# Kernel optimization log

Hardware: AMD Instinct MI355X
Metric: run time of the kernel (lower is better)

The kernel has to match this reference:

```python
import jax, jax.numpy as jnp
import numpy as np

N = 100_000   # nodes
E = 1_000_000 # edges
F = 128       # nfeat
H = 2         # heads
C = 64        # nhid (per-head out channels)
NEG_SLOPE = 0.2
BN_EPS = 1e-5


def setup_inputs() -> dict:
    key = jax.random.key(0)
    ks = jax.random.split(key, 6)
    x = jax.random.normal(ks[0], (N, F), dtype=jnp.float32)
    edge_index = jax.random.randint(ks[1], (2, E), 0, N, dtype=jnp.int32)
    # GATConv params (xavier-ish scale)
    W = jax.random.normal(ks[2], (F, H * C), dtype=jnp.float32) * np.float32(1.0 / np.sqrt(F))
    att_src = jax.random.normal(ks[3], (H, C), dtype=jnp.float32) * np.float32(0.1)
    att_dst = jax.random.normal(ks[4], (H, C), dtype=jnp.float32) * np.float32(0.1)
    bias = jnp.zeros((H * C,), dtype=jnp.float32)
    # BatchNorm1d affine params
    gamma = jnp.ones((H * C,), dtype=jnp.float32)
    beta = jnp.zeros((H * C,), dtype=jnp.float32)
    return {"x": x, "edge_index": edge_index, "W": W, "att_src": att_src,
            "att_dst": att_dst, "bias": bias, "gamma": gamma, "beta": beta}


def reference(x, edge_index, W, att_src, att_dst, bias, gamma, beta):
    n = x.shape[0]
    # --- GATConv (PyG semantics): add self-loops, per-head linear, edge attention ---
    loop = jnp.arange(n, dtype=edge_index.dtype)
    src = jnp.concatenate([edge_index[0], loop])  # message sources (j)
    dst = jnp.concatenate([edge_index[1], loop])  # aggregation targets (i)

    h = (x @ W).reshape(n, H, C)                      # [N,H,C]
    a_src = jnp.einsum('nhc,hc->nh', h, att_src)      # [N,H]
    a_dst = jnp.einsum('nhc,hc->nh', h, att_dst)      # [N,H]

    e = jax.nn.leaky_relu(a_src[src] + a_dst[dst], NEG_SLOPE)  # [Et,H]
    # segment softmax over incoming edges of each dst node
    m = jax.lax.stop_gradient(jax.ops.segment_max(e, dst, num_segments=n))
    e = jnp.exp(e - m[dst])
    s = jax.ops.segment_sum(e, dst, num_segments=n)
    alpha = e / s[dst]                                 # [Et,H]

    out = jax.ops.segment_sum(alpha[:, :, None] * h[src], dst, num_segments=n)  # [N,H,C]
    out = out.reshape(n, H * C) + bias                 # concat heads + bias

    # --- transition: ReLU -> BatchNorm1d (training-mode batch stats) -> Dropout(eval=identity) ---
    out = jax.nn.relu(out)
    mean = out.mean(axis=0)
    var = out.var(axis=0)  # biased, as BN uses for normalization
    out = gamma * (out - mean) * jax.lax.rsqrt(var + BN_EPS) + beta
    return out
```

## Files before the change

### kernel.cpp

```cpp
#include <hip/hip_runtime.h>

#define NN 100000
#define EE 1000000
#define ET (EE + NN)
#define HC 128
#define NB 391
#define AGG_BLOCKS 2048
#define NGRP (NN / 4)
#define NTILE 6250
#define GEMM_BLKS 768

typedef __attribute__((ext_vector_type(8))) short short8;
typedef __attribute__((ext_vector_type(4))) float f32x4;

__device__ __forceinline__ unsigned cvtpk(float a, float b) {
    unsigned r;
    asm("v_cvt_pk_bf16_f32 %0, %1, %2" : "=v"(r) : "v"(a), "v"(b));
    return r;
}

__global__ __launch_bounds__(256) void k_gemmhist(
    const float* __restrict__ x, const float* __restrict__ W,
    const float* __restrict__ atts, const float* __restrict__ attd,
    unsigned* __restrict__ hB, float2* __restrict__ asrc2, float2* __restrict__ adst2,
    const int* __restrict__ ei, int* __restrict__ hist)
{
    __shared__ uint4 wl[2048];

    if (blockIdx.x >= GEMM_BLKS) {
        const int t0 = (blockIdx.x - GEMM_BLKS) * 256 + threadIdx.x;
        for (int t = t0; t < ET; t += 256 * 256) {
            int d = (t < EE) ? ei[EE + t] : (t - EE);
            atomicAdd(&hist[d], 1);
        }
        return;
    }

    for (int i = threadIdx.x; i < 2048; i += 256) {
        const int bid = i >> 6, l = i & 63;
        const int ks = bid >> 3, nt = bid & 7;
        const int n = nt * 16 + (l & 15);
        const int k0 = ks * 32 + (l >> 4) * 8;
        wl[i] = make_uint4(cvtpk(W[(k0 + 0) * HC + n], W[(k0 + 1) * HC + n]),
                           cvtpk(W[(k0 + 2) * HC + n], W[(k0 + 3) * HC + n]),
                           cvtpk(W[(k0 + 4) * HC + n], W[(k0 + 5) * HC + n]),
                           cvtpk(W[(k0 + 6) * HC + n], W[(k0 + 7) * HC + n]));
    }
    __syncthreads();

    const int wv = threadIdx.x >> 6, lane = threadIdx.x & 63;
    const int g = lane >> 4, c15 = lane & 15;

    float As[8], Ad[8];
    #pragma unroll
    for (int nt = 0; nt < 8; ++nt) {
        As[nt] = atts[nt * 16 + c15];
        Ad[nt] = attd[nt * 16 + c15];
    }

    for (int t = blockIdx.x * 4 + wv; t < NTILE; t += GEMM_BLKS * 4) {
        const int row0 = t * 16;
        union { unsigned u[4]; short8 v; } af[4];
        const float* xr = x + (size_t)(row0 + c15) * HC + g * 8;
        #pragma unroll
        for (int ks = 0; ks < 4; ++ks) {
            float4 lo = *(const float4*)(xr + ks * 32);
            float4 hi = *(const float4*)(xr + ks * 32 + 4);
            af[ks].u[0] = cvtpk(lo.x, lo.y);
            af[ks].u[1] = cvtpk(lo.z, lo.w);
            af[ks].u[2] = cvtpk(hi.x, hi.y);
            af[ks].u[3] = cvtpk(hi.z, hi.w);
        }
        f32x4 acc[8];
        #pragma unroll
        for (int nt = 0; nt < 8; ++nt) acc[nt] = (f32x4)(0.f);
        #pragma unroll
        for (int nt = 0; nt < 8; ++nt) {
            #pragma unroll
            for (int ks = 0; ks < 4; ++ks) {
                short8 bfr = *(const short8*)&wl[(ks * 8 + nt) * 64 + lane];
                acc[nt] = __builtin_amdgcn_mfma_f32_16x16x32_bf16(
                    af[ks].v, bfr, acc[nt], 0, 0, 0);
            }
        }
        #pragma unroll
        for (int r = 0; r < 4; ++r) {
            const int row = row0 + g * 4 + r;
            float ps = 0.f, pd = 0.f, qs = 0.f, qd = 0.f;
            #pragma unroll
            for (int nt = 0; nt < 4; ++nt) {
                float a = acc[nt][r], b = acc[nt + 4][r];
                hB[(size_t)row * 64 + nt * 16 + c15] = cvtpk(a, b);
                ps += a * As[nt];     qs += a * Ad[nt];
                pd += b * As[nt + 4]; qd += b * Ad[nt + 4];
            }
            for (int off = 8; off; off >>= 1) {
                ps += __shfl_xor(ps, off); pd += __shfl_xor(pd, off);
                qs += __shfl_xor(qs, off); qd += __shfl_xor(qd, off);
            }
            if (c15 == 0) {
                asrc2[row] = make_float2(ps, pd);
                adst2[row] = make_float2(qs, qd);
            }
        }
    }
}

__device__ __forceinline__ void edge_sd(const int* __restrict__ ei, int t, int& s, int& d) {
    if (t < EE) { s = ei[t]; d = ei[EE + t]; }
    else        { s = t - EE; d = t - EE; }
}

__global__ __launch_bounds__(256) void k_scan1(const int* __restrict__ hist,
                                               int* __restrict__ part)
{
    __shared__ int ls[256];
    int i = blockIdx.x * 256 + threadIdx.x;
    ls[threadIdx.x] = (i < NN) ? hist[i] : 0;
    __syncthreads();
    for (int off = 128; off; off >>= 1) {
        if (threadIdx.x < off) ls[threadIdx.x] += ls[threadIdx.x + off];
        __syncthreads();
    }
    if (!threadIdx.x) part[blockIdx.x] = ls[0];
}

__global__ __launch_bounds__(256) void k_scan3(const int* __restrict__ hist,
                                               const int* __restrict__ part,
                                               int* __restrict__ row_ptr)
{
    __shared__ int ls[256];
    __shared__ int bofs[NB];
    const int tid = threadIdx.x;
    if (tid < 64) {
        int carry = 0;
        for (int c = 0; c < NB; c += 64) {
            const int idx = c + tid;
            int v = (idx < NB) ? part[idx] : 0;
            const int orig = v;
            for (int o = 1; o < 64; o <<= 1) {
                int u = __shfl_up(v, o);
                if (tid >= o) v += u;
            }
            if (idx < NB) bofs[idx] = carry + v - orig;
            carry += __shfl(v, 63);
        }
    }
    int i = blockIdx.x * 256 + tid;
    int v = (i < NN) ? hist[i] : 0;
    ls[tid] = v;
    __syncthreads();
    for (int off = 1; off < 256; off <<= 1) {
        int t = (tid >= off) ? ls[tid - off] : 0;
        __syncthreads();
        ls[tid] += t;
        __syncthreads();
    }
    if (i < NN) row_ptr[i] = bofs[blockIdx.x] + ls[tid] - v;
    if (i == 0) row_ptr[NN] = ET;
}

__global__ __launch_bounds__(256) void k_bucket(
    const int* __restrict__ ei, const float* __restrict__ asrc,
    const float* __restrict__ adst, const int* __restrict__ row_ptr,
    int* __restrict__ cursor, uint2* __restrict__ csr8)
{
    int t = blockIdx.x * 256 + threadIdx.x;
    if (t >= ET) return;
    int s, d; edge_sd(ei, t, s, d);
    float2 av = *(const float2*)&asrc[s * 2];
    float2 dv = *(const float2*)&adst[d * 2];
    float e0 = av.x + dv.x; e0 = e0 > 0.f ? e0 : 0.2f * e0;
    float e1 = av.y + dv.y; e1 = e1 > 0.f ? e1 : 0.2f * e1;
    int pos = row_ptr[d] + atomicAdd(&cursor[d], 1);
    csr8[pos] = make_uint2((unsigned)s, cvtpk(__expf(e0), __expf(e1)));
}

__device__ __forceinline__ void gather8x2(const unsigned* base, const unsigned* off,
                                          unsigned long long* w) {
    asm volatile(
        "global_load_dwordx2 %0, %8,  %16\n\t"
        "global_load_dwordx2 %1, %9,  %16\n\t"
        "global_load_dwordx2 %2, %10, %16\n\t"
        "global_load_dwordx2 %3, %11, %16\n\t"
        "global_load_dwordx2 %4, %12, %16\n\t"
        "global_load_dwordx2 %5, %13, %16\n\t"
        "global_load_dwordx2 %6, %14, %16\n\t"
        "global_load_dwordx2 %7, %15, %16\n\t"
        "s_waitcnt vmcnt(0)"
        : "=&v"(w[0]), "=&v"(w[1]), "=&v"(w[2]), "=&v"(w[3]),
          "=&v"(w[4]), "=&v"(w[5]), "=&v"(w[6]), "=&v"(w[7])
        : "v"(off[0]), "v"(off[1]), "v"(off[2]), "v"(off[3]),
          "v"(off[4]), "v"(off[5]), "v"(off[6]), "v"(off[7]),
          "s"(base)
        : "memory");
}

__global__ __launch_bounds__(256) void k_agg(
    const int* __restrict__ row_ptr, const uint2* __restrict__ csr8,
    const unsigned* __restrict__ hB, const float* __restrict__ bias,
    float* __restrict__ out, float* __restrict__ bpart)
{
    __shared__ float lsum[HC], lsq[HC];
    __shared__ int    lidx[4][64];
    __shared__ float2 lp[4][64];
    const int tid = threadIdx.x;
    if (tid < HC) { lsum[tid] = 0.f; lsq[tid] = 0.f; }
    __syncthreads();

    const int wv = tid >> 6, lane = tid & 63;
    const int half = lane >> 5, m = lane & 31;
    const float bA0 = bias[2*m],      bB0 = bias[2*m + 1];
    const float bA1 = bias[2*m + 64], bB1 = bias[2*m + 65];

    for (int g = blockIdx.x; g < NGRP; g += AGG_BLOCKS) {
        const int node = g * 4 + wv;
        const int beg = row_ptr[node], end = row_ptr[node + 1];

        float s0 = 0.f, s1 = 0.f;
        float a0 = 0.f, a1 = 0.f, b0 = 0.f, b1 = 0.f;

        for (int base = beg; base < end; base += 64) {
            const int cnt = min(64, end - base);
            if (lane < cnt) {
                uint2 e = csr8[base + lane];
                float2 pv = make_float2(__uint_as_float(e.y << 16),
                                        __uint_as_float(e.y & 0xffff0000u));
                lidx[wv][lane] = (int)e.x;
                lp[wv][lane] = pv;
                s0 += pv.x; s1 += pv.y;
            }
            for (int j0 = 0; j0 < cnt; j0 += 16) {
                unsigned off[8]; unsigned long long w[8];
                float px[8], py[8];
                #pragma unroll
                for (int u = 0; u < 8; ++u) {
                    int j  = j0 + 2 * u + half;
                    int jc = j < cnt ? j : cnt - 1;
                    int s  = lidx[wv][jc];
                    float2 pv = lp[wv][jc];
                    px[u] = j < cnt ? pv.x : 0.f;
                    py[u] = j < cnt ? pv.y : 0.f;
                    off[u] = ((unsigned)s * 64u + (unsigned)m * 2u) * 4u;
                }
                gather8x2(hB, off, w);
                #pragma unroll
                for (int u = 0; u < 8; ++u) {
                    unsigned wlo = (unsigned)w[u];
                    unsigned whi = (unsigned)(w[u] >> 32);
                    a0 = fmaf(px[u], __uint_as_float(wlo << 16),          a0);
                    a1 = fmaf(py[u], __uint_as_float(wlo & 0xffff0000u),  a1);
                    b0 = fmaf(px[u], __uint_as_float(whi << 16),          b0);
                    b1 = fmaf(py[u], __uint_as_float(whi & 0xffff0000u),  b1);
                }
            }
        }

        a0 += __shfl_xor(a0, 32); a1 += __shfl_xor(a1, 32);
        b0 += __shfl_xor(b0, 32); b1 += __shfl_xor(b1, 32);
        for (int o = 32; o; o >>= 1) {
            s0 += __shfl_xor(s0, o);
            s1 += __shfl_xor(s1, o);
        }
        const float i0 = 1.f / s0, i1 = 1.f / s1;

        if (half == 0) {
            float vA0 = a0 * i0 + bA0; vA0 = vA0 > 0.f ? vA0 : 0.f;
            float vB0 = b0 * i0 + bB0; vB0 = vB0 > 0.f ? vB0 : 0.f;
            float vA1 = a1 * i1 + bA1; vA1 = vA1 > 0.f ? vA1 : 0.f;
            float vB1 = b1 * i1 + bB1; vB1 = vB1 > 0.f ? vB1 : 0.f;
            *(float2*)&out[(size_t)node * HC + 2*m]      = make_float2(vA0, vB0);
            *(float2*)&out[(size_t)node * HC + 64 + 2*m] = make_float2(vA1, vB1);
            atomicAdd(&lsum[2*m],      vA0); atomicAdd(&lsq[2*m],      vA0 * vA0);
            atomicAdd(&lsum[2*m + 1],  vB0); atomicAdd(&lsq[2*m + 1],  vB0 * vB0);
            atomicAdd(&lsum[2*m + 64], vA1); atomicAdd(&lsq[2*m + 64], vA1 * vA1);
            atomicAdd(&lsum[2*m + 65], vB1); atomicAdd(&lsq[2*m + 65], vB1 * vB1);
        }
    }

    __syncthreads();
    bpart[(size_t)blockIdx.x * 256 + tid] = tid < HC ? lsum[tid] : lsq[tid - HC];
}

__global__ __launch_bounds__(256) void k_red(const float* __restrict__ bpart,
                                             float* __restrict__ p2)
{
    const int tid = threadIdx.x;
    float acc = 0.f;
    const int r0 = blockIdx.x * (AGG_BLOCKS / 16);
    #pragma unroll 4
    for (int r = 0; r < AGG_BLOCKS / 16; ++r)
        acc += bpart[(size_t)(r0 + r) * 256 + tid];
    p2[blockIdx.x * 256 + tid] = acc;
}

__global__ __launch_bounds__(256) void k_apply(
    const float* __restrict__ p2, const float* __restrict__ gamma,
    const float* __restrict__ beta, float* __restrict__ out)
{
    __shared__ float scsh[256];
    const int tid = threadIdx.x;
    if (tid < HC) {
        float sum = 0.f, sq = 0.f;
        #pragma unroll
        for (int i = 0; i < 16; ++i) {
            sum += p2[i * 256 + tid];
            sq  += p2[i * 256 + tid + 128];
        }
        float mean = sum * (1.f / NN);
        float var  = sq * (1.f / NN) - mean * mean;
        float sc   = gamma[tid] * rsqrtf(var + 1e-5f);
        scsh[tid]       = sc;
        scsh[128 + tid] = beta[tid] - mean * sc;
    }
    __syncthreads();
    for (size_t i = (size_t)blockIdx.x * 256 + tid; i < (size_t)NN * HC / 4;
         i += (size_t)gridDim.x * 256) {
        float4 v = ((float4*)out)[i];
        int c = (int)((i * 4) & (HC - 1));
        v.x = v.x * scsh[c]     + scsh[128 + c];
        v.y = v.y * scsh[c + 1] + scsh[128 + c + 1];
        v.z = v.z * scsh[c + 2] + scsh[128 + c + 2];
        v.w = v.w * scsh[c + 3] + scsh[128 + c + 3];
        ((float4*)out)[i] = v;
    }
}

extern "C" void kernel_launch(void* const* d_in, const int* in_sizes, int n_in,
                              void* d_out, int out_size, void* d_ws, size_t ws_size,
                              hipStream_t stream) {
    const float* x     = (const float*)d_in[0];
    const int*   ei    = (const int*)  d_in[1];
    const float* W     = (const float*)d_in[2];
    const float* atts  = (const float*)d_in[3];
    const float* attd  = (const float*)d_in[4];
    const float* bias  = (const float*)d_in[5];
    const float* gamma = (const float*)d_in[6];
    const float* beta  = (const float*)d_in[7];
    float* out = (float*)d_out;
    float* ws  = (float*)d_ws;

    unsigned* hB     = (unsigned*)ws;
    float*    asrc   = ws + 6400000;
    float*    adst   = ws + 6600000;
    int*      hist   = (int*)(ws + 6800000);
    int*      cursor = (int*)(ws + 6900000);
    int*      row_ptr= (int*)(ws + 7000512);
    int*      part   = (int*)(ws + 7100513);
    uint2*    csr8   = (uint2*)(ws + 7101026);
    float*    bpart  = ws + 9301026;
    float*    p2     = ws + 9825314;

    hipMemsetAsync(hist, 0, (size_t)200000 * sizeof(int), stream);

    k_gemmhist<<<1024, 256, 0, stream>>>(x, W, atts, attd, hB,
                                         (float2*)asrc, (float2*)adst, ei, hist);
    k_scan1   <<<NB, 256, 0, stream>>>(hist, part);
    k_scan3   <<<NB, 256, 0, stream>>>(hist, part, row_ptr);
    k_bucket  <<<(ET + 255) / 256, 256, 0, stream>>>(ei, asrc, adst, row_ptr,
                                                     cursor, csr8);
    k_agg     <<<AGG_BLOCKS, 256, 0, stream>>>(row_ptr, csr8, hB, bias,
                                               out, bpart);
    k_red     <<<16, 256, 0, stream>>>(bpart, p2);
    k_apply   <<<2048, 256, 0, stream>>>(p2, gamma, beta, out);
}
```

Before: 299.5 us.

## Precompute attention logits via folded W·att and overlap GEMM with bucketing

The attention logits are computed directly from x using precomputed vectors W·att_src and W·att_dst, so the first kernel only needs a per-node matrix-vector product plus the histogram. The bf16 MFMA GEMM that writes h moves into the bucketing kernel, where some blocks run the GEMM while others scatter edges into the CSR. The aim is to overlap the GEMM with the atomic-heavy bucketing pass instead of running it alongside the histogram. In exchange, x is read twice, and the logits now come from fp32 x·(W·att) rather than the bf16-rounded h path.

```diff
diff --git a/kernel.cpp b/kernel.cpp
--- a/kernel.cpp
+++ b/kernel.cpp
@@ -8,7 +8,8 @@
 #define AGG_BLOCKS 2048
 #define NGRP (NN / 4)
 #define NTILE 6250
-#define GEMM_BLKS 768
+#define PRE_MV 391
+#define GB_GEMM 640
 
 typedef __attribute__((ext_vector_type(8))) short short8;
 typedef __attribute__((ext_vector_type(4))) float f32x4;
@@ -19,16 +20,19 @@
     return r;
 }
 
-__global__ __launch_bounds__(256) void k_gemmhist(
+__device__ __forceinline__ void edge_sd(const int* __restrict__ ei, int t, int& s, int& d) {
+    if (t < EE) { s = ei[t]; d = ei[EE + t]; }
+    else        { s = t - EE; d = t - EE; }
+}
+
+__global__ __launch_bounds__(256) void k_pre(
     const float* __restrict__ x, const float* __restrict__ W,
     const float* __restrict__ atts, const float* __restrict__ attd,
-    unsigned* __restrict__ hB, float2* __restrict__ asrc2, float2* __restrict__ adst2,
+    float2* __restrict__ asrc2, float2* __restrict__ adst2,
     const int* __restrict__ ei, int* __restrict__ hist)
 {
-    __shared__ uint4 wl[2048];
-
-    if (blockIdx.x >= GEMM_BLKS) {
-        const int t0 = (blockIdx.x - GEMM_BLKS) * 256 + threadIdx.x;
+    if (blockIdx.x >= PRE_MV) {
+        const int t0 = (blockIdx.x - PRE_MV) * 256 + threadIdx.x;
         for (int t = t0; t < ET; t += 256 * 256) {
             int d = (t < EE) ? ei[EE + t] : (t - EE);
             atomicAdd(&hist[d], 1);
@@ -36,79 +40,38 @@
         return;
     }
 
-    for (int i = threadIdx.x; i < 2048; i += 256) {
-        const int bid = i >> 6, l = i & 63;
-        const int ks = bid >> 3, nt = bid & 7;
-        const int n = nt * 16 + (l & 15);
-        const int k0 = ks * 32 + (l >> 4) * 8;
-        wl[i] = make_uint4(cvtpk(W[(k0 + 0) * HC + n], W[(k0 + 1) * HC + n]),
-                           cvtpk(W[(k0 + 2) * HC + n], W[(k0 + 3) * HC + n]),
-                           cvtpk(W[(k0 + 4) * HC + n], W[(k0 + 5) * HC + n]),
-                           cvtpk(W[(k0 + 6) * HC + n], W[(k0 + 7) * HC + n]));
-    }
-    __syncthreads();
-
-    const int wv = threadIdx.x >> 6, lane = threadIdx.x & 63;
-    const int g = lane >> 4, c15 = lane & 15;
-
-    float As[8], Ad[8];
-    #pragma unroll
-    for (int nt = 0; nt < 8; ++nt) {
-        As[nt] = atts[nt * 16 + c15];
-        Ad[nt] = attd[nt * 16 + c15];
-    }
-
-    for (int t = blockIdx.x * 4 + wv; t < NTILE; t += GEMM_BLKS * 4) {
-        const int row0 = t * 16;
-        union { unsigned u[4]; short8 v; } af[4];
-        const float* xr = x + (size_t)(row0 + c15) * HC + g * 8;
-        #pragma unroll
-        for (int ks = 0; ks < 4; ++ks) {
-            float4 lo = *(const float4*)(xr + ks * 32);
-            float4 hi = *(const float4*)(xr + ks * 32 + 4);
-            af[ks].u[0] = cvtpk(lo.x, lo.y);
-            af[ks].u[1] = cvtpk(lo.z, lo.w);
-            af[ks].u[2] = cvtpk(hi.x, hi.y);
-            af[ks].u[3] = cvtpk(hi.z, hi.w);
-        }
-        f32x4 acc[8];
-        #pragma unroll
-        for (int nt = 0; nt < 8; ++nt) acc[nt] = (f32x4)(0.f);
-        #pragma unroll
-        for (int nt = 0; nt < 8; ++nt) {
-            #pragma unroll
-            for (int ks = 0; ks < 4; ++ks) {
-                short8 bfr = *(const short8*)&wl[(ks * 8 + nt) * 64 + lane];
-                acc[nt] = __builtin_amdgcn_mfma_f32_16x16x32_bf16(
-                    af[ks].v, bfr, acc[nt], 0, 0, 0);
-            }
-        }
-        #pragma unroll
-        for (int r = 0; r < 4; ++r) {
-            const int row = row0 + g * 4 + r;
-            float ps = 0.f, pd = 0.f, qs = 0.f, qd = 0.f;
-            #pragma unroll
-            for (int nt = 0; nt < 4; ++nt) {
-                float a = acc[nt][r], b = acc[nt + 4][r];
-                hB[(size_t)row * 64 + nt * 16 + c15] = cvtpk(a, b);
-                ps += a * As[nt];     qs += a * Ad[nt];
-                pd += b * As[nt + 4]; qd += b * Ad[nt + 4];
-            }
-            for (int off = 8; off; off >>= 1) {
-                ps += __shfl_xor(ps, off); pd += __shfl_xor(pd, off);
-                qs += __shfl_xor(qs, off); qd += __shfl_xor(qd, off);
-            }
-            if (c15 == 0) {
-                asrc2[row] = make_float2(ps, pd);
-                adst2[row] = make_float2(qs, qd);
-            }
-        }
-    }
-}
-
-__device__ __forceinline__ void edge_sd(const int* __restrict__ ei, int t, int& s, int& d) {
-    if (t < EE) { s = ei[t]; d = ei[EE + t]; }
-    else        { s = t - EE; d = t - EE; }
+    __shared__ float v0[HC], v1[HC], u0[HC], u1[HC];
+    const int tid = threadIdx.x;
+    if (tid < HC) {
+        float a0 = 0.f, a1 = 0.f, b0 = 0.f, b1 = 0.f;
+        const float* wr = W + tid * HC;
+        #pragma unroll 8
+        for (int c = 0; c < 64; ++c) {
+            float wlo = wr[c], whi = wr[64 + c];
+            a0 = fmaf(wlo, atts[c],      a0);
+            a1 = fmaf(whi, atts[64 + c], a1);
+            b0 = fmaf(wlo, attd[c],      b0);
+            b1 = fmaf(whi, attd[64 + c], b1);
+        }
+        v0[tid] = a0; v1[tid] = a1; u0[tid] = b0; u1[tid] = b1;
+    }
+    __syncthreads();
+
+    const int node = blockIdx.x * 256 + tid;
+    if (node >= NN) return;
+    const float* xr = x + (size_t)node * HC;
+    float as0 = 0.f, as1 = 0.f, ad0 = 0.f, ad1 = 0.f;
+    #pragma unroll 4
+    for (int k4 = 0; k4 < HC / 4; ++k4) {
+        float4 xv = *(const float4*)(xr + k4 * 4);
+        const int k = k4 * 4;
+        as0 = fmaf(xv.x, v0[k], fmaf(xv.y, v0[k+1], fmaf(xv.z, v0[k+2], fmaf(xv.w, v0[k+3], as0))));
+        as1 = fmaf(xv.x, v1[k], fmaf(xv.y, v1[k+1], fmaf(xv.z, v1[k+2], fmaf(xv.w, v1[k+3], as1))));
+        ad0 = fmaf(xv.x, u0[k], fmaf(xv.y, u0[k+1], fmaf(xv.z, u0[k+2], fmaf(xv.w, u0[k+3], ad0))));
+        ad1 = fmaf(xv.x, u1[k], fmaf(xv.y, u1[k+1], fmaf(xv.z, u1[k+2], fmaf(xv.w, u1[k+3], ad1))));
+    }
+    asrc2[node] = make_float2(as0, as1);
+    adst2[node] = make_float2(ad0, ad1);
 }
 
 __global__ __launch_bounds__(256) void k_scan1(const int* __restrict__ hist,
@@ -160,20 +123,77 @@
     if (i == 0) row_ptr[NN] = ET;
 }
 
-__global__ __launch_bounds__(256) void k_bucket(
-    const int* __restrict__ ei, const float* __restrict__ asrc,
-    const float* __restrict__ adst, const int* __restrict__ row_ptr,
+__global__ __launch_bounds__(256) void k_gemmbucket(
+    const float* __restrict__ x, const float* __restrict__ W,
+    unsigned* __restrict__ hB,
+    const int* __restrict__ ei, const float2* __restrict__ asrc2,
+    const float2* __restrict__ adst2, const int* __restrict__ row_ptr,
     int* __restrict__ cursor, uint2* __restrict__ csr8)
 {
-    int t = blockIdx.x * 256 + threadIdx.x;
-    if (t >= ET) return;
-    int s, d; edge_sd(ei, t, s, d);
-    float2 av = *(const float2*)&asrc[s * 2];
-    float2 dv = *(const float2*)&adst[d * 2];
-    float e0 = av.x + dv.x; e0 = e0 > 0.f ? e0 : 0.2f * e0;
-    float e1 = av.y + dv.y; e1 = e1 > 0.f ? e1 : 0.2f * e1;
-    int pos = row_ptr[d] + atomicAdd(&cursor[d], 1);
-    csr8[pos] = make_uint2((unsigned)s, cvtpk(__expf(e0), __expf(e1)));
+    __shared__ uint4 wl[2048];
+
+    if (blockIdx.x >= GB_GEMM) {
+        const int t0 = (blockIdx.x - GB_GEMM) * 256 + threadIdx.x;
+        for (int t = t0; t < ET; t += (1024 - GB_GEMM) * 256) {
+            int s, d; edge_sd(ei, t, s, d);
+            float2 av = asrc2[s];
+            float2 dv = adst2[d];
+            float e0 = av.x + dv.x; e0 = e0 > 0.f ? e0 : 0.2f * e0;
+            float e1 = av.y + dv.y; e1 = e1 > 0.f ? e1 : 0.2f * e1;
+            int pos = row_ptr[d] + atomicAdd(&cursor[d], 1);
+            csr8[pos] = make_uint2((unsigned)s, cvtpk(__expf(e0), __expf(e1)));
+        }
+        return;
+    }
+
+    for (int i = threadIdx.x; i < 2048; i += 256) {
+        const int bid = i >> 6, l = i & 63;
+        const int ks = bid >> 3, nt = bid & 7;
+        const int n = nt * 16 + (l & 15);
+        const int k0 = ks * 32 + (l >> 4) * 8;
+        wl[i] = make_uint4(cvtpk(W[(k0 + 0) * HC + n], W[(k0 + 1) * HC + n]),
+                           cvtpk(W[(k0 + 2) * HC + n], W[(k0 + 3) * HC + n]),
+                           cvtpk(W[(k0 + 4) * HC + n], W[(k0 + 5) * HC + n]),
+                           cvtpk(W[(k0 + 6) * HC + n], W[(k0 + 7) * HC + n]));
+    }
+    __syncthreads();
+
+    const int wv = threadIdx.x >> 6, lane = threadIdx.x & 63;
+    const int g = lane >> 4, c15 = lane & 15;
+
+    for (int t = blockIdx.x * 4 + wv; t < NTILE; t += GB_GEMM * 4) {
+        const int row0 = t * 16;
+        union { unsigned u[4]; short8 v; } af[4];
+        const float* xr = x + (size_t)(row0 + c15) * HC + g * 8;
+        #pragma unroll
+        for (int ks = 0; ks < 4; ++ks) {
+            float4 lo = *(const float4*)(xr + ks * 32);
+            float4 hi = *(const float4*)(xr + ks * 32 + 4);
+            af[ks].u[0] = cvtpk(lo.x, lo.y);
+            af[ks].u[1] = cvtpk(lo.z, lo.w);
+            af[ks].u[2] = cvtpk(hi.x, hi.y);
+            af[ks].u[3] = cvtpk(hi.z, hi.w);
+        }
+        f32x4 acc[8];
+        #pragma unroll
+        for (int nt = 0; nt < 8; ++nt) acc[nt] = (f32x4)(0.f);
+        #pragma unroll
+        for (int nt = 0; nt < 8; ++nt) {
+            #pragma unroll
+            for (int ks = 0; ks < 4; ++ks) {
+                short8 bfr = *(const short8*)&wl[(ks * 8 + nt) * 64 + lane];
+                acc[nt] = __builtin_amdgcn_mfma_f32_16x16x32_bf16(
+                    af[ks].v, bfr, acc[nt], 0, 0, 0);
+            }
+        }
+        #pragma unroll
+        for (int r = 0; r < 4; ++r) {
+            const int row = row0 + g * 4 + r;
+            #pragma unroll
+            for (int nt = 0; nt < 4; ++nt)
+                hB[(size_t)row * 64 + nt * 16 + c15] = cvtpk(acc[nt][r], acc[nt + 4][r]);
+        }
+    }
 }
 
 __device__ __forceinline__ void gather8x2(const unsigned* base, const unsigned* off,
@@ -353,14 +373,16 @@
 
     hipMemsetAsync(hist, 0, (size_t)200000 * sizeof(int), stream);
 
-    k_gemmhist<<<1024, 256, 0, stream>>>(x, W, atts, attd, hB,
-                                         (float2*)asrc, (float2*)adst, ei, hist);
-    k_scan1   <<<NB, 256, 0, stream>>>(hist, part);
-    k_scan3   <<<NB, 256, 0, stream>>>(hist, part, row_ptr);
-    k_bucket  <<<(ET + 255) / 256, 256, 0, stream>>>(ei, asrc, adst, row_ptr,
-                                                     cursor, csr8);
-    k_agg     <<<AGG_BLOCKS, 256, 0, stream>>>(row_ptr, csr8, hB, bias,
-                                               out, bpart);
-    k_red     <<<16, 256, 0, stream>>>(bpart, p2);
-    k_apply   <<<2048, 256, 0, stream>>>(p2, gamma, beta, out);
-}
+    k_pre       <<<PRE_MV + 256, 256, 0, stream>>>(x, W, atts, attd,
+                                                   (float2*)asrc, (float2*)adst,
+                                                   ei, hist);
+    k_scan1     <<<NB, 256, 0, stream>>>(hist, part);
+    k_scan3     <<<NB, 256, 0, stream>>>(hist, part, row_ptr);
+    k_gemmbucket<<<1024, 256, 0, stream>>>(x, W, hB, ei,
+                                           (const float2*)asrc, (const float2*)adst,
+                                           row_ptr, cursor, csr8);
+    k_agg       <<<AGG_BLOCKS, 256, 0, stream>>>(row_ptr, csr8, hB, bias,
+                                                 out, bpart);
+    k_red       <<<16, 256, 0, stream>>>(bpart, p2);
+    k_apply     <<<2048, 256, 0, stream>>>(p2, gamma, beta, out);
+}
```

New measurement: 309.9 us, median of 2. 1.03x slower.
